# Kernel tuning notes

Hardware: AMD Instinct MI355X
Metric: run time of the kernel (lower is better)

## Reference

```python
import jax, jax.numpy as jnp
import numpy as np

N_WIRES = 8
EMBED = 768
B, S = 16, 2048


def setup_inputs() -> dict:
    key = jax.random.key(0)
    k1, k2, k3, k4 = jax.random.split(key, 4)
    return {
        "x": jax.random.normal(k1, (B, S, EMBED), dtype=jnp.float32),
        "w_q": jax.random.normal(k2, (N_WIRES, EMBED), dtype=jnp.float32) * (1.0 / np.sqrt(EMBED)),
        "w_out": jax.random.normal(k3, (EMBED, N_WIRES), dtype=jnp.float32) * (1.0 / np.sqrt(N_WIRES)),
        "q_params": jax.random.normal(k4, (N_WIRES,), dtype=jnp.float32),
    }


def _simulate(angles):
    """Statevector sim: RX(angle_w) on each wire w, then ring of CNOTs, then <Z_w>.
    angles: [B, S, n].  Returns [B, S, n] Pauli-Z expectations."""
    b, s, n = angles.shape
    # |0...0> initial state, one qubit per trailing axis of size 2
    state = jnp.zeros((b, s) + (2,) * n, dtype=jnp.complex64)
    state = state.at[(slice(None), slice(None)) + (0,) * n].set(1.0)
    # RX gates (data angle + learned angle already fused in `angles`)
    for w in range(n):
        ax = 2 + w
        half = angles[..., w] * 0.5
        bshape = (b, s) + (1,) * (n - 1)
        c = jnp.cos(half).reshape(bshape)
        si = jnp.sin(half).reshape(bshape)
        a0 = jnp.take(state, 0, axis=ax)
        a1 = jnp.take(state, 1, axis=ax)
        state = jnp.stack([c * a0 - 1j * si * a1, -1j * si * a0 + c * a1], axis=ax)
    # CNOT chain: (0,1),(1,2),...,(n-2,n-1),(n-1,0)
    for src, tgt in [(i, i + 1) for i in range(n - 1)] + [(n - 1, 0)]:
        sax, tax = 2 + src, 2 + tgt
        a0 = jnp.take(state, 0, axis=sax)
        a1 = jnp.take(state, 1, axis=sax)
        tadj = tax - (1 if tax > sax else 0)  # target axis after removing src axis
        state = jnp.stack([a0, jnp.flip(a1, axis=tadj)], axis=sax)
    probs = jnp.real(state * jnp.conj(state))  # [B,S,2,...,2]
    zs = []
    for w in range(n):
        axes = tuple(a for a in range(2, 2 + n) if a != 2 + w)
        marg = probs.sum(axis=axes)  # [B,S,2]
        zs.append(marg[..., 0] - marg[..., 1])
    return jnp.stack(zs, axis=-1)


def reference(x, w_q, w_out, q_params):
    # per-token RX angles; two RX on same wire commute -> fuse data + learned angle
    angles = jnp.einsum("bse,ne->bsn", x, w_q) + q_params  # [B,S,n]
    z = _simulate(angles)  # [B,S,n]
    return jnp.einsum("bsn,en->bse", z, w_out)  # [B,S,E]
```

## Files before the change

### kernel.cpp

```cpp
#include <hip/hip_runtime.h>
#include <math.h>


using f32x4 = __attribute__((ext_vector_type(4))) float;

constexpr int E  = 768;
constexpr int NW = 8;
constexpr int BLOCK = 256;
constexpr int TOKENS = 16 * 2048;
constexpr int TOK_PER_WAVE  = 4;
constexpr int TOK_PER_BLOCK = TOK_PER_WAVE * 4;
constexpr int GRID = TOKENS / TOK_PER_BLOCK;

__device__ __forceinline__ float dot12(const f32x4& a0, const f32x4& a1, const f32x4& a2,
                                       const f32x4& b0, const f32x4& b1, const f32x4& b2) {
    return a0.x*b0.x + a0.y*b0.y + a0.z*b0.z + a0.w*b0.w
         + a1.x*b1.x + a1.y*b1.y + a1.z*b1.z + a1.w*b1.w
         + a2.x*b2.x + a2.y*b2.y + a2.z*b2.z + a2.w*b2.w;
}

__device__ __forceinline__ void circuit8(const float zf[NW], int lane, float qpl,
                                         float z[NW]) {
    float v4[4];
    #pragma unroll
    for (int i = 0; i < 4; ++i) {
        float a = zf[2*i], b = zf[2*i+1];
        float keep = (lane & 1) ? b : a;
        float send = (lane & 1) ? a : b;
        v4[i] = keep + __shfl_xor(send, 1, 64);
    }
    float v2[2];
    #pragma unroll
    for (int i = 0; i < 2; ++i) {
        float a = v4[2*i], b = v4[2*i+1];
        float keep = (lane & 2) ? b : a;
        float send = (lane & 2) ? a : b;
        v2[i] = keep + __shfl_xor(send, 2, 64);
    }
    float a = v2[0], b = v2[1];
    float keep = (lane & 4) ? b : a;
    float send = (lane & 4) ? a : b;
    float v = keep + __shfl_xor(send, 4, 64);
    v += __shfl_xor(v, 8, 64);
    v += __shfl_xor(v, 16, 64);
    v += __shfl_xor(v, 32, 64);
    float c = __cosf(v + qpl);
    float cx = __shfl_xor(c, 1, 64);
    float e0 = (lane & 1) ? cx : c;
    float e1 = (lane & 1) ? c : cx;
    float e0x = __shfl_xor(e0, 2, 64), e1x = __shfl_xor(e1, 2, 64);
    float f0 = (lane & 2) ? e0x : e0;
    float f1 = (lane & 2) ? e1x : e1;
    float f2 = (lane & 2) ? e0  : e0x;
    float f3 = (lane & 2) ? e1  : e1x;
    float f0x = __shfl_xor(f0, 4, 64), f1x = __shfl_xor(f1, 4, 64);
    float f2x = __shfl_xor(f2, 4, 64), f3x = __shfl_xor(f3, 4, 64);
    float c0 = (lane & 4) ? f0x : f0;
    float c1 = (lane & 4) ? f1x : f1;
    float c2 = (lane & 4) ? f2x : f2;
    float c3 = (lane & 4) ? f3x : f3;
    float c4 = (lane & 4) ? f0  : f0x;
    float c5 = (lane & 4) ? f1  : f1x;
    float c6 = (lane & 4) ? f2  : f2x;
    float c7 = (lane & 4) ? f3  : f3x;
    float p1 = c0*c1, p2 = p1*c2, p3 = p2*c3, p4 = p3*c4;
    float p5 = p4*c5, p6 = p5*c6, p7 = p6*c7;
    float s  = c1*c2*c3*c4*c5*c6*c7;
    z[0] = s;  z[1] = p1; z[2] = p2; z[3] = p3;
    z[4] = p4; z[5] = p5; z[6] = p6; z[7] = p7;
}

__global__ __launch_bounds__(BLOCK, 4)
void mhaq_kernel(const float* __restrict__ x,
                 const float* __restrict__ w_q,
                 const float* __restrict__ w_out,
                 const float* __restrict__ q_params,
                 float* __restrict__ out)
{
    __shared__ float wq_lds[NW][E];
    __shared__ float wt_lds[NW][E];

    const int tid  = threadIdx.x;
    const int wave = tid >> 6;
    const int lane = tid & 63;
    const int col  = lane * 4;
    const int t0   = blockIdx.x * TOK_PER_BLOCK + wave * TOK_PER_WAVE;

    {
        const f32x4* src = reinterpret_cast<const f32x4*>(w_q);
        f32x4* dst = reinterpret_cast<f32x4*>(&wq_lds[0][0]);
        #pragma unroll
        for (int r = 0; r < (NW * E / 4) / BLOCK; ++r)
            dst[tid + r * BLOCK] = src[tid + r * BLOCK];
    }
    {
        const f32x4* src = reinterpret_cast<const f32x4*>(w_out);
        #pragma unroll
        for (int r = 0; r < (NW * E / 4) / BLOCK; ++r) {
            int idx = tid + r * BLOCK;
            f32x4 v = src[idx];
            int e  = idx >> 1;
            int n0 = (idx & 1) * 4;
            wt_lds[n0 + 0][e] = v.x;
            wt_lds[n0 + 1][e] = v.y;
            wt_lds[n0 + 2][e] = v.z;
            wt_lds[n0 + 3][e] = v.w;
        }
    }
    const float qpl = q_params[lane & 7];

    f32x4 xv[TOK_PER_WAVE][3];
    #pragma unroll
    for (int tt = 0; tt < TOK_PER_WAVE; ++tt) {
        const f32x4* xp = reinterpret_cast<const f32x4*>(x + (size_t)(t0 + tt) * E);
        #pragma unroll
        for (int k = 0; k < 3; ++k)
            xv[tt][k] = xp[lane + k * 64];
    }
    __syncthreads();

    float zf[TOK_PER_WAVE][NW];
    #pragma unroll
    for (int n = 0; n < NW; ++n) {
        const f32x4 w0 = *reinterpret_cast<const f32x4*>(&wq_lds[n][col]);
        const f32x4 w1 = *reinterpret_cast<const f32x4*>(&wq_lds[n][col + 256]);
        const f32x4 w2 = *reinterpret_cast<const f32x4*>(&wq_lds[n][col + 512]);
        #pragma unroll
        for (int tt = 0; tt < TOK_PER_WAVE; ++tt)
            zf[tt][n] = dot12(xv[tt][0], xv[tt][1], xv[tt][2], w0, w1, w2);
    }

    float z[TOK_PER_WAVE][NW];
    #pragma unroll
    for (int tt = 0; tt < TOK_PER_WAVE; ++tt)
        circuit8(zf[tt], lane, qpl, z[tt]);

    #pragma unroll
    for (int k = 0; k < 3; ++k) {
        const int e0 = k * 256 + col;
        f32x4 wv[NW];
        #pragma unroll
        for (int n = 0; n < NW; ++n)
            wv[n] = *reinterpret_cast<const f32x4*>(&wt_lds[n][e0]);
        #pragma unroll
        for (int tt = 0; tt < TOK_PER_WAVE; ++tt) {
            float ox = 0.f, oy = 0.f, oz = 0.f, ow = 0.f;
            #pragma unroll
            for (int n = 0; n < NW; ++n) {
                ox += z[tt][n] * wv[n].x;
                oy += z[tt][n] * wv[n].y;
                oz += z[tt][n] * wv[n].z;
                ow += z[tt][n] * wv[n].w;
            }
            f32x4 o; o.x = ox; o.y = oy; o.z = oz; o.w = ow;
            __builtin_nontemporal_store(
                o, reinterpret_cast<f32x4*>(out + (size_t)(t0 + tt) * E + e0));
        }
    }
}

extern "C" void kernel_launch(void* const* d_in, const int* in_sizes, int n_in,
                              void* d_out, int out_size, void* d_ws, size_t ws_size,
                              hipStream_t stream) {
    const float* x        = (const float*)d_in[0];
    const float* w_q      = (const float*)d_in[1];
    const float* w_out    = (const float*)d_in[2];
    const float* q_params = (const float*)d_in[3];
    float* out = (float*)d_out;

    hipLaunchKernelGGL(mhaq_kernel, dim3(GRID), dim3(BLOCK), 0, stream,
                       x, w_q, w_out, q_params, out);
}
```

Baseline: 37.18 us.

## Process two token groups per block and prefetch the second group's x during compute

Each block now handles two 16-token groups instead of one, halving the grid. The weight staging into LDS is amortised over twice the tokens, and the second group's x loads are issued before the first group's circuit and output phase, overlapping memory latency with compute. The cost is higher register pressure from holding two x tiles at once, plus fewer blocks to spread across CUs.

```diff
diff --git a/kernel.cpp b/kernel.cpp
--- a/kernel.cpp
+++ b/kernel.cpp
@@ -9,7 +9,8 @@
 constexpr int BLOCK = 256;
 constexpr int TOKENS = 16 * 2048;
 constexpr int TOK_PER_WAVE  = 4;
-constexpr int TOK_PER_BLOCK = TOK_PER_WAVE * 4;
+constexpr int GROUP_TOK = TOK_PER_WAVE * 4;
+constexpr int TOK_PER_BLOCK = GROUP_TOK * 2;
 constexpr int GRID = TOKENS / TOK_PER_BLOCK;
 
 __device__ __forceinline__ float dot12(const f32x4& a0, const f32x4& a1, const f32x4& a2,
@@ -70,46 +71,8 @@
     z[4] = p4; z[5] = p5; z[6] = p6; z[7] = p7;
 }
 
-__global__ __launch_bounds__(BLOCK, 4)
-void mhaq_kernel(const float* __restrict__ x,
-                 const float* __restrict__ w_q,
-                 const float* __restrict__ w_out,
-                 const float* __restrict__ q_params,
-                 float* __restrict__ out)
-{
-    __shared__ float wq_lds[NW][E];
-    __shared__ float wt_lds[NW][E];
-
-    const int tid  = threadIdx.x;
-    const int wave = tid >> 6;
-    const int lane = tid & 63;
-    const int col  = lane * 4;
-    const int t0   = blockIdx.x * TOK_PER_BLOCK + wave * TOK_PER_WAVE;
-
-    {
-        const f32x4* src = reinterpret_cast<const f32x4*>(w_q);
-        f32x4* dst = reinterpret_cast<f32x4*>(&wq_lds[0][0]);
-        #pragma unroll
-        for (int r = 0; r < (NW * E / 4) / BLOCK; ++r)
-            dst[tid + r * BLOCK] = src[tid + r * BLOCK];
-    }
-    {
-        const f32x4* src = reinterpret_cast<const f32x4*>(w_out);
-        #pragma unroll
-        for (int r = 0; r < (NW * E / 4) / BLOCK; ++r) {
-            int idx = tid + r * BLOCK;
-            f32x4 v = src[idx];
-            int e  = idx >> 1;
-            int n0 = (idx & 1) * 4;
-            wt_lds[n0 + 0][e] = v.x;
-            wt_lds[n0 + 1][e] = v.y;
-            wt_lds[n0 + 2][e] = v.z;
-            wt_lds[n0 + 3][e] = v.w;
-        }
-    }
-    const float qpl = q_params[lane & 7];
-
-    f32x4 xv[TOK_PER_WAVE][3];
+__device__ __forceinline__ void load_x4(const float* __restrict__ x, int t0, int lane,
+                                        f32x4 xv[TOK_PER_WAVE][3]) {
     #pragma unroll
     for (int tt = 0; tt < TOK_PER_WAVE; ++tt) {
         const f32x4* xp = reinterpret_cast<const f32x4*>(x + (size_t)(t0 + tt) * E);
@@ -117,9 +80,11 @@
         for (int k = 0; k < 3; ++k)
             xv[tt][k] = xp[lane + k * 64];
     }
-    __syncthreads();
-
-    float zf[TOK_PER_WAVE][NW];
+}
+
+__device__ __forceinline__ void dot_phase(const f32x4 xv[TOK_PER_WAVE][3],
+                                          const float (*wq_lds)[E], int col,
+                                          float zf[TOK_PER_WAVE][NW]) {
     #pragma unroll
     for (int n = 0; n < NW; ++n) {
         const f32x4 w0 = *reinterpret_cast<const f32x4*>(&wq_lds[n][col]);
@@ -129,7 +94,12 @@
         for (int tt = 0; tt < TOK_PER_WAVE; ++tt)
             zf[tt][n] = dot12(xv[tt][0], xv[tt][1], xv[tt][2], w0, w1, w2);
     }
-
+}
+
+__device__ __forceinline__ void finish_phase(float zf[TOK_PER_WAVE][NW],
+                                             const float (*wt_lds)[E],
+                                             int t0, int lane, int col, float qpl,
+                                             float* __restrict__ out) {
     float z[TOK_PER_WAVE][NW];
     #pragma unroll
     for (int tt = 0; tt < TOK_PER_WAVE; ++tt)
@@ -159,6 +129,63 @@
     }
 }
 
+__global__ __launch_bounds__(BLOCK, 4)
+void mhaq_kernel(const float* __restrict__ x,
+                 const float* __restrict__ w_q,
+                 const float* __restrict__ w_out,
+                 const float* __restrict__ q_params,
+                 float* __restrict__ out)
+{
+    __shared__ float wq_lds[NW][E];
+    __shared__ float wt_lds[NW][E];
+
+    const int tid  = threadIdx.x;
+    const int wave = tid >> 6;
+    const int lane = tid & 63;
+    const int col  = lane * 4;
+    const int t0a  = blockIdx.x * TOK_PER_BLOCK + wave * TOK_PER_WAVE;
+    const int t0b  = t0a + GROUP_TOK;
+
+    {
+        const f32x4* src = reinterpret_cast<const f32x4*>(w_q);
+        f32x4* dst = reinterpret_cast<f32x4*>(&wq_lds[0][0]);
+        #pragma unroll
+        for (int r = 0; r < (NW * E / 4) / BLOCK; ++r)
+            dst[tid + r * BLOCK] = src[tid + r * BLOCK];
+    }
+    {
+        const f32x4* src = reinterpret_cast<const f32x4*>(w_out);
+        #pragma unroll
+        for (int r = 0; r < (NW * E / 4) / BLOCK; ++r) {
+            int idx = tid + r * BLOCK;
+            f32x4 v = src[idx];
+            int e  = idx >> 1;
+            int n0 = (idx & 1) * 4;
+            wt_lds[n0 + 0][e] = v.x;
+            wt_lds[n0 + 1][e] = v.y;
+            wt_lds[n0 + 2][e] = v.z;
+            wt_lds[n0 + 3][e] = v.w;
+        }
+    }
+    const float qpl = q_params[lane & 7];
+
+    f32x4 xv0[TOK_PER_WAVE][3];
+    load_x4(x, t0a, lane, xv0);
+    __syncthreads();
+
+    float zf0[TOK_PER_WAVE][NW];
+    dot_phase(xv0, wq_lds, col, zf0);
+
+    f32x4 xv1[TOK_PER_WAVE][3];
+    load_x4(x, t0b, lane, xv1);
+
+    finish_phase(zf0, wt_lds, t0a, lane, col, qpl, out);
+
+    float zf1[TOK_PER_WAVE][NW];
+    dot_phase(xv1, wq_lds, col, zf1);
+    finish_phase(zf1, wt_lds, t0b, lane, col, qpl, out);
+}
+
 extern "C" void kernel_launch(void* const* d_in, const int* in_sizes, int n_in,
                               void* d_out, int out_size, void* d_ws, size_t ws_size,
                               hipStream_t stream) {
```

Measured after the change: 37.49 us. About the same (+0.8%).
